# Kernel tuning notes

Measured on AMD Instinct MI355X. Metric: run time of the kernel, lower is better.

Reference implementation:

```python
import jax, jax.numpy as jnp
import numpy as np

B, N, F, H, D = 2, 2048, 1024, 16, 64


def setup_inputs() -> dict:
    key = jax.random.key(0)
    ks = jax.random.split(key, 5)
    s = 0.02
    return {
        "x": jax.random.normal(ks[0], (B, N, F), jnp.float32),
        "w_qkv": (jax.random.normal(ks[1], (3 * H * D, F), jnp.float32) * s),
        "w_out": (jax.random.normal(ks[2], (F, H * D), jnp.float32) * s),
        "w_hp_pre": (jax.random.normal(ks[3], (H, H), jnp.float32) * (1.0 / H)),
        "b_hp_pre": jnp.zeros((H,), jnp.float32),
        "w_hp_post": (jax.random.normal(ks[4], (H, H), jnp.float32) * (1.0 / H)),
        "b_hp_post": jnp.zeros((H,), jnp.float32),
    }


def reference(x, w_qkv, w_out, w_hp_pre, b_hp_pre, w_hp_post, b_hp_post):
    b, n, f = x.shape
    # qkv projection; rearrange 'b n (h d qkv) -> qkv b h n d' (qkv innermost)
    proj = (x @ w_qkv.T).reshape(b, n, H, D, 3)
    q = jnp.transpose(proj[..., 0], (0, 2, 1, 3))  # b h n d
    k = jnp.transpose(proj[..., 1], (0, 2, 1, 3))
    v = jnp.transpose(proj[..., 2], (0, 2, 1, 3))
    kv = jnp.stack([k, v], axis=0)  # (2, b, h, n, d) -- returned cache

    scale = D ** -0.5
    dots = jnp.einsum('bhid,bhjd->bhij', q, k) * scale
    # pre talking-heads: 1x1 conv over head channel
    dots = jnp.einsum('gh,bhij->bgij', w_hp_pre, dots) + b_hp_pre[None, :, None, None]
    attn = jax.nn.softmax(dots, axis=-1)
    # post talking-heads
    attn = jnp.einsum('gh,bhij->bgij', w_hp_post, attn) + b_hp_post[None, :, None, None]
    out = jnp.einsum('bhij,bhjd->bhid', attn, v)
    out = jnp.transpose(out, (0, 2, 1, 3)).reshape(b, n, H * D)
    out = out @ w_out.T
    return out, kv
```

## Files before the change

kernel.cpp:

```cpp
#include <hip/hip_runtime.h>
#include <hip/hip_bf16.h>
#include <cstdint>
#include <cstddef>

#define B_ 2
#define N_ 2048
#define F_ 1024
#define H_ 16
#define D_ 64

typedef float f32x4 __attribute__((ext_vector_type(4)));
typedef short s16x8 __attribute__((ext_vector_type(8)));
typedef short s16x4 __attribute__((ext_vector_type(4)));

__device__ __forceinline__ unsigned short f2bf(float f) {
  union { __hip_bfloat16 h; unsigned short u; } c;
  c.h = __float2bfloat16(f);
  return c.u;
}

__device__ __forceinline__ void bar_lgkm() {
  asm volatile("s_waitcnt lgkmcnt(0)" ::: "memory");
  __builtin_amdgcn_s_barrier();
}

__global__ __launch_bounds__(256) void cvt_bf16(const float* __restrict__ in,
                                                unsigned short* __restrict__ out,
                                                int n8) {
  const int t = blockIdx.x * 256 + threadIdx.x;
  if (t >= n8) return;
  const float4* p = (const float4*)in + (size_t)t * 2;
  float4 a = p[0], b = p[1];
  s16x8 o;
  o[0] = f2bf(a.x); o[1] = f2bf(a.y); o[2] = f2bf(a.z); o[3] = f2bf(a.w);
  o[4] = f2bf(b.x); o[5] = f2bf(b.y); o[6] = f2bf(b.z); o[7] = f2bf(b.w);
  *((s16x8*)out + t) = o;
}

__global__ __launch_bounds__(256) void cvt_wqkv_perm(const float* __restrict__ in,
                                                     unsigned short* __restrict__ out) {
  const int t = blockIdx.x * 256 + threadIdx.x;
  const int rowp = t >> 7;
  const int kk = (t & 127) * 8;
  const int c = rowp >> 10, rem = rowp & 1023;
  const int h = rem >> 6, d = rem & 63;
  const float* p = in + (size_t)(h * 192 + d * 3 + c) * 1024 + kk;
  float4 a = *(const float4*)p, b = *(const float4*)(p + 4);
  s16x8 o;
  o[0] = f2bf(a.x); o[1] = f2bf(a.y); o[2] = f2bf(a.z); o[3] = f2bf(a.w);
  o[4] = f2bf(b.x); o[5] = f2bf(b.y); o[6] = f2bf(b.z); o[7] = f2bf(b.w);
  *((s16x8*)&out[(size_t)rowp * 1024 + kk]) = o;
}

__global__ __launch_bounds__(256) void cvt_sum4(const float* __restrict__ a,
                                                unsigned short* __restrict__ out) {
  const int t = blockIdx.x * 256 + threadIdx.x;
  const size_t stride = (size_t)B_ * N_ * 1024 / 4;
  float4 x0 = *((const float4*)a + t);
  float4 x1 = *((const float4*)a + stride + t);
  float4 x2 = *((const float4*)a + 2 * stride + t);
  float4 x3 = *((const float4*)a + 3 * stride + t);
  s16x4 o;
  o[0] = f2bf((x0.x + x1.x) + (x2.x + x3.x));
  o[1] = f2bf((x0.y + x1.y) + (x2.y + x3.y));
  o[2] = f2bf((x0.z + x1.z) + (x2.z + x3.z));
  o[3] = f2bf((x0.w + x1.w) + (x2.w + x3.w));
  *((s16x4*)out + t) = o;
}

template <int MODE>
__global__ __launch_bounds__(256) void gemm_bf16(const unsigned short* __restrict__ A,
                                                 const unsigned short* __restrict__ W,
                                                 float* __restrict__ o0,
                                                 unsigned short* __restrict__ oQ,
                                                 unsigned short* __restrict__ oK,
                                                 unsigned short* __restrict__ oVt) {
  __shared__ unsigned short As[128 * 72];
  __shared__ unsigned short Bs[128 * 72];
  const int m0 = blockIdx.y * 128, c0 = blockIdx.x * 128;
  const int tid = threadIdx.x;
  const int wave = tid >> 6, lane = tid & 63;
  const int wm = (wave & 1) * 64, wn = (wave >> 1) * 64;
  const int lm = lane & 15, lq = lane >> 4;
  f32x4 acc[4][4] = {};
  for (int k0 = 0; k0 < 1024; k0 += 64) {
#pragma unroll
    for (int it = 0; it < 4; ++it) {
      const int chunk = it * 256 + tid;
      const int row = chunk >> 3, kq = (chunk & 7) * 8;
      *(float4*)&As[row * 72 + kq] = *(const float4*)&A[(size_t)(m0 + row) * 1024 + k0 + kq];
      *(float4*)&Bs[row * 72 + kq] = *(const float4*)&W[(size_t)(c0 + row) * 1024 + k0 + kq];
    }
    __syncthreads();
#pragma unroll
    for (int ks = 0; ks < 2; ++ks) {
      s16x8 af[4], bfr[4];
#pragma unroll
      for (int i = 0; i < 4; ++i) {
        af[i] = *(const s16x8*)&As[(wm + i * 16 + lm) * 72 + ks * 32 + lq * 8];
        bfr[i] = *(const s16x8*)&Bs[(wn + i * 16 + lm) * 72 + ks * 32 + lq * 8];
      }
#pragma unroll
      for (int i = 0; i < 4; ++i)
#pragma unroll
        for (int j = 0; j < 4; ++j)
          acc[i][j] = __builtin_amdgcn_mfma_f32_16x16x32_bf16(af[i], bfr[j], acc[i][j], 0, 0, 0);
    }
    __syncthreads();
  }
  if (MODE == 1) {
#pragma unroll
    for (int i = 0; i < 4; ++i)
#pragma unroll
      for (int j = 0; j < 4; ++j)
#pragma unroll
        for (int r = 0; r < 4; ++r) {
          const int m = m0 + wm + i * 16 + lq * 4 + r;
          const int col = c0 + wn + j * 16 + lm;
          o0[(size_t)m * 1024 + col] = acc[i][j][r];
        }
  } else {
    const int cls = blockIdx.x >> 3;
    const int colbase = (blockIdx.x & 7) * 128;
    if (cls == 0) {
#pragma unroll
      for (int i = 0; i < 4; ++i)
#pragma unroll
        for (int j = 0; j < 4; ++j) {
          const int cl = colbase + wn + j * 16 + lm;
          const int h = cl >> 6, d = cl & 63;
#pragma unroll
          for (int r = 0; r < 4; ++r) {
            const int m = m0 + wm + i * 16 + lq * 4 + r;
            const int bb = m >> 11, n = m & 2047;
            oQ[(((size_t)bb * H_ + h) * N_ + n) * D_ + d] = f2bf(acc[i][j][r]);
          }
        }
    } else if (cls == 1) {
#pragma unroll
      for (int i = 0; i < 4; ++i)
#pragma unroll
        for (int j = 0; j < 4; ++j) {
          const int cl = colbase + wn + j * 16 + lm;
          const int h = cl >> 6, d = cl & 63;
#pragma unroll
          for (int r = 0; r < 4; ++r) {
            const int m = m0 + wm + i * 16 + lq * 4 + r;
            const int bb = m >> 11, n = m & 2047;
            const size_t idx = (((size_t)bb * H_ + h) * N_ + n) * D_ + d;
            o0[idx] = acc[i][j][r];
            oK[idx] = f2bf(acc[i][j][r]);
          }
        }
    } else {
#pragma unroll
      for (int i = 0; i < 4; ++i) {
        const int n0 = m0 + wm + i * 16 + lq * 4;
        const int bb = n0 >> 11, nl = n0 & 2047;
#pragma unroll
        for (int j = 0; j < 4; ++j) {
          const int cl = colbase + wn + j * 16 + lm;
          const int h = cl >> 6, d = cl & 63;
          s16x4 vp;
#pragma unroll
          for (int r = 0; r < 4; ++r) {
            const size_t idx = (((size_t)bb * H_ + h) * N_ + nl + r) * D_ + d;
            o0[(size_t)B_ * H_ * N_ * D_ + idx] = acc[i][j][r];
            vp[r] = (short)f2bf(acc[i][j][r]);
          }
          *(s16x4*)&oVt[(((size_t)bb * H_ + h) * D_ + d) * N_ + nl] = vp;
        }
      }
    }
  }
}

#define SS_J 20
#define SLOT 320
#define SS_I 644
#define SS_TOT (32 * SS_I + 16)
#define PS_J 36
#define PS_G 1156

__global__ __launch_bounds__(512, 4) void attn_l(const unsigned short* __restrict__ Qb,
                                                 const unsigned short* __restrict__ Kb,
                                                 const float* __restrict__ wpre,
                                                 const float* __restrict__ bpre,
                                                 float* __restrict__ l_glob) {
  __shared__ unsigned short Ssh[SS_TOT];
  const int tid = threadIdx.x;
  const int wave = tid >> 6, lane = tid & 63;
  const int lm = lane & 15, lq = lane >> 4;
  const int b = blockIdx.z, jh = blockIdx.y;
  const int i0 = blockIdx.x * 32;
  const int j00 = jh * 512;
  const int h0 = wave * 2;

  for (int t = tid; t < SS_TOT; t += 512) Ssh[t] = 0;

  s16x8 aq[2][2][2];
#pragma unroll
  for (int hh = 0; hh < 2; ++hh)
#pragma unroll
    for (int mi = 0; mi < 2; ++mi)
#pragma unroll
      for (int ks = 0; ks < 2; ++ks)
        aq[hh][mi][ks] = *(const s16x8*)&Qb[(((size_t)(b * H_ + h0 + hh) * N_) + i0 + mi * 16 + lm) * D_ + ks * 32 + lq * 8];

  s16x8 apre;
#pragma unroll
  for (int t = 0; t < 8; ++t) apre[t] = 0;
  if (lq < 2)
#pragma unroll
    for (int t = 0; t < 8; ++t) apre[t] = (short)f2bf(wpre[lm * 16 + lq * 8 + t] * 0.125f);
  float bpre_r[4];
#pragma unroll
  for (int r = 0; r < 4; ++r) bpre_r[r] = bpre[lq * 4 + r];

  float lacc[4][4] = {};

  for (int js = 0; js < 512; js += 32) {
    const int j0 = j00 + js;
    s16x8 kr[2][2][2];
#pragma unroll
    for (int jt = 0; jt < 2; ++jt)
#pragma unroll
      for (int hh = 0; hh < 2; ++hh) {
        const unsigned short* kp = &Kb[(((size_t)(b * H_ + h0 + hh) * N_) + j0 + jt * 16 + lm) * D_ + lq * 8];
        kr[jt][hh][0] = *(const s16x8*)kp;
        kr[jt][hh][1] = *(const s16x8*)(kp + 32);
      }
    bar_lgkm();
#pragma unroll
    for (int jt = 0; jt < 2; ++jt) {
      f32x4 c[2][2];
#pragma unroll
      for (int hh = 0; hh < 2; ++hh)
#pragma unroll
        for (int mi = 0; mi < 2; ++mi) {
          f32x4 cc = {};
          cc = __builtin_amdgcn_mfma_f32_16x16x32_bf16(aq[hh][mi][0], kr[jt][hh][0], cc, 0, 0, 0);
          cc = __builtin_amdgcn_mfma_f32_16x16x32_bf16(aq[hh][mi][1], kr[jt][hh][1], cc, 0, 0, 0);
          c[hh][mi] = cc;
        }
#pragma unroll
      for (int mi = 0; mi < 2; ++mi)
#pragma unroll
        for (int r = 0; r < 4; ++r) {
          unsigned int pk = (unsigned int)f2bf(c[0][mi][r]) | ((unsigned int)f2bf(c[1][mi][r]) << 16);
          *(unsigned int*)&Ssh[(mi * 16 + lq * 4 + r) * SS_I + jt * SLOT + lm * SS_J + h0] = pk;
        }
    }
    bar_lgkm();
#pragma unroll
    for (int jt = 0; jt < 2; ++jt) {
      s16x4 p0[4], p1[4];
#pragma unroll
      for (int u = 0; u < 4; ++u) {
        const unsigned short* srow = &Ssh[(wave * 4 + u) * SS_I + jt * SLOT + lm * SS_J + lq * 8];
        p0[u] = *(const s16x4*)srow;
        p1[u] = *(const s16x4*)(srow + 4);
      }
#pragma unroll
      for (int u = 0; u < 4; ++u) {
        s16x8 bs;
        bs[0] = p0[u][0]; bs[1] = p0[u][1]; bs[2] = p0[u][2]; bs[3] = p0[u][3];
        bs[4] = p1[u][0]; bs[5] = p1[u][1]; bs[6] = p1[u][2]; bs[7] = p1[u][3];
        f32x4 c = {};
        c = __builtin_amdgcn_mfma_f32_16x16x32_bf16(apre, bs, c, 0, 0, 0);
#pragma unroll
        for (int r = 0; r < 4; ++r) lacc[u][r] += __expf(c[r] + bpre_r[r]);
      }
    }
  }
#pragma unroll
  for (int ig = 0; ig < 4; ++ig)
#pragma unroll
    for (int r = 0; r < 4; ++r) {
      float v = lacc[ig][r];
      v += __shfl_xor(v, 1); v += __shfl_xor(v, 2);
      v += __shfl_xor(v, 4); v += __shfl_xor(v, 8);
      if (lm == 0)
        atomicAdd(&l_glob[((size_t)b * N_ + i0 + wave * 4 + ig) * H_ + lq * 4 + r], v);
    }
}

__global__ __launch_bounds__(512, 2) void attn_av(const unsigned short* __restrict__ Qb,
                                                  const unsigned short* __restrict__ Kb,
                                                  const unsigned short* __restrict__ Vt,
                                                  const float* __restrict__ wpre,
                                                  const float* __restrict__ bpre,
                                                  const float* __restrict__ wpost,
                                                  const float* __restrict__ bpost,
                                                  const float* __restrict__ l_glob,
                                                  float* __restrict__ Opart) {
  __shared__ unsigned short Ssh[SS_TOT];
  __shared__ unsigned short Psh[16 * PS_G];
  __shared__ float linv[512];
  const int tid = threadIdx.x;
  const int wave = tid >> 6, lane = tid & 63;
  const int lm = lane & 15, lq = lane >> 4;
  const int b = blockIdx.z, jh = blockIdx.y;
  const int i0 = blockIdx.x * 32;
  const int j00 = jh * 512;
  const int h0 = wave * 2;
  float* Oout = Opart + (size_t)jh * ((size_t)B_ * N_ * 1024);

  for (int t = tid; t < SS_TOT; t += 512) Ssh[t] = 0;
  linv[tid] = 1.0f / l_glob[((size_t)b * N_ + i0 + (tid >> 4)) * H_ + (tid & 15)];

  s16x8 aq[2][2][2];
#pragma unroll
  for (int hh = 0; hh < 2; ++hh)
#pragma unroll
    for (int mi = 0; mi < 2; ++mi)
#pragma unroll
      for (int ks = 0; ks < 2; ++ks)
        aq[hh][mi][ks] = *(const s16x8*)&Qb[(((size_t)(b * H_ + h0 + hh) * N_) + i0 + mi * 16 + lm) * D_ + ks * 32 + lq * 8];

  s16x8 apre, apost;
#pragma unroll
  for (int t = 0; t < 8; ++t) { apre[t] = 0; apost[t] = 0; }
  if (lq < 2)
#pragma unroll
    for (int t = 0; t < 8; ++t) {
      apre[t] = (short)f2bf(wpre[lm * 16 + lq * 8 + t] * 0.125f);
      apost[t] = (short)f2bf(wpost[lm * 16 + lq * 8 + t]);
    }
  float bpre_r[4];
#pragma unroll
  for (int r = 0; r < 4; ++r) bpre_r[r] = bpre[lq * 4 + r];
  const float bpost_lm = bpost[lm];

  __syncthreads();

  float lifs[4][4];
#pragma unroll
  for (int u = 0; u < 4; ++u)
#pragma unroll
    for (int r = 0; r < 4; ++r)
      lifs[u][r] = linv[(wave * 4 + u) * 16 + lq * 4 + r];

  f32x4 acc[2][2][4] = {};

  for (int js = 0; js < 512; js += 32) {
    const int j0 = j00 + js;
    s16x8 kr[2][2][2];
#pragma unroll
    for (int jt = 0; jt < 2; ++jt)
#pragma unroll
      for (int hh = 0; hh < 2; ++hh) {
        const unsigned short* kp = &Kb[(((size_t)(b * H_ + h0 + hh) * N_) + j0 + jt * 16 + lm) * D_ + lq * 8];
        kr[jt][hh][0] = *(const s16x8*)kp;
        kr[jt][hh][1] = *(const s16x8*)(kp + 32);
      }
    s16x8 vtreg[2][4];
#pragma unroll
    for (int g = 0; g < 2; ++g)
#pragma unroll
      for (int nd = 0; nd < 4; ++nd)
        vtreg[g][nd] = *(const s16x8*)&Vt[(((size_t)(b * H_ + h0 + g) * D_) + nd * 16 + lm) * N_ + j0 + lq * 8];
#pragma unroll
    for (int jt = 0; jt < 2; ++jt) {
      f32x4 c[2][2];
#pragma unroll
      for (int hh = 0; hh < 2; ++hh)
#pragma unroll
        for (int mi = 0; mi < 2; ++mi) {
          f32x4 cc = {};
          cc = __builtin_amdgcn_mfma_f32_16x16x32_bf16(aq[hh][mi][0], kr[jt][hh][0], cc, 0, 0, 0);
          cc = __builtin_amdgcn_mfma_f32_16x16x32_bf16(aq[hh][mi][1], kr[jt][hh][1], cc, 0, 0, 0);
          c[hh][mi] = cc;
        }
#pragma unroll
      for (int mi = 0; mi < 2; ++mi)
#pragma unroll
        for (int r = 0; r < 4; ++r) {
          unsigned int pk = (unsigned int)f2bf(c[0][mi][r]) | ((unsigned int)f2bf(c[1][mi][r]) << 16);
          *(unsigned int*)&Ssh[(mi * 16 + lq * 4 + r) * SS_I + jt * SLOT + lm * SS_J + h0] = pk;
        }
    }
    bar_lgkm();
#pragma unroll
    for (int jt = 0; jt < 2; ++jt) {
      s16x4 p0[4], p1[4];
#pragma unroll
      for (int u = 0; u < 4; ++u) {
        const unsigned short* srow = &Ssh[(wave * 4 + u) * SS_I + jt * SLOT + lm * SS_J + lq * 8];
        p0[u] = *(const s16x4*)srow;
        p1[u] = *(const s16x4*)(srow + 4);
      }
      f32x4 cpre[4];
#pragma unroll
      for (int u = 0; u < 4; ++u) {
        s16x8 bs;
        bs[0] = p0[u][0]; bs[1] = p0[u][1]; bs[2] = p0[u][2]; bs[3] = p0[u][3];
        bs[4] = p1[u][0]; bs[5] = p1[u][1]; bs[6] = p1[u][2]; bs[7] = p1[u][3];
        f32x4 c = {};
        cpre[u] = __builtin_amdgcn_mfma_f32_16x16x32_bf16(apre, bs, c, 0, 0, 0);
      }
#pragma unroll
      for (int u = 0; u < 4; ++u) {
        unsigned short* srow = &Ssh[(wave * 4 + u) * SS_I + jt * SLOT];
        s16x4 ep;
#pragma unroll
        for (int r = 0; r < 4; ++r)
          ep[r] = (short)f2bf(__expf(cpre[u][r] + bpre_r[r]) * lifs[u][r]);
        *(s16x4*)(srow + lm * SS_J + lq * 4) = ep;
      }
      s16x4 q0[4], q1[4];
#pragma unroll
      for (int u = 0; u < 4; ++u) {
        const unsigned short* srow = &Ssh[(wave * 4 + u) * SS_I + jt * SLOT + lm * SS_J + lq * 8];
        q0[u] = *(const s16x4*)srow;
        q1[u] = *(const s16x4*)(srow + 4);
      }
#pragma unroll
      for (int u = 0; u < 4; ++u) {
        s16x8 be;
        be[0] = q0[u][0]; be[1] = q0[u][1]; be[2] = q0[u][2]; be[3] = q0[u][3];
        be[4] = q1[u][0]; be[5] = q1[u][1]; be[6] = q1[u][2]; be[7] = q1[u][3];
        f32x4 c2 = {};
        c2 = __builtin_amdgcn_mfma_f32_16x16x32_bf16(be, apost, c2, 0, 0, 0);
        s16x4 pv;
#pragma unroll
        for (int r = 0; r < 4; ++r) pv[r] = (short)f2bf(c2[r] + bpost_lm);
        *(s16x4*)&Psh[lm * PS_G + (wave * 4 + u) * PS_J + jt * 16 + lq * 4] = pv;
      }
    }
    bar_lgkm();
    s16x8 ap[2][2];
#pragma unroll
    for (int g = 0; g < 2; ++g)
#pragma unroll
      for (int mi = 0; mi < 2; ++mi) {
        const unsigned short* pb = &Psh[(h0 + g) * PS_G + (mi * 16 + lm) * PS_J + lq * 8];
        s16x4 a0 = *(const s16x4*)pb;
        s16x4 a1 = *(const s16x4*)(pb + 4);
        s16x8 t;
        t[0] = a0[0]; t[1] = a0[1]; t[2] = a0[2]; t[3] = a0[3];
        t[4] = a1[0]; t[5] = a1[1]; t[6] = a1[2]; t[7] = a1[3];
        ap[g][mi] = t;
      }
#pragma unroll
    for (int g = 0; g < 2; ++g)
#pragma unroll
      for (int mi = 0; mi < 2; ++mi)
#pragma unroll
        for (int nd = 0; nd < 4; ++nd)
          acc[g][mi][nd] = __builtin_amdgcn_mfma_f32_16x16x32_bf16(ap[g][mi], vtreg[g][nd], acc[g][mi][nd], 0, 0, 0);
  }
#pragma unroll
  for (int g = 0; g < 2; ++g)
#pragma unroll
    for (int mi = 0; mi < 2; ++mi)
#pragma unroll
      for (int nd = 0; nd < 4; ++nd)
#pragma unroll
        for (int r = 0; r < 4; ++r)
          Oout[((size_t)b * N_ + i0 + mi * 16 + lq * 4 + r) * 1024 + (h0 + g) * 64 + nd * 16 + lm] = acc[g][mi][nd][r];
}

extern "C" void kernel_launch(void* const* d_in, const int* in_sizes, int n_in,
                              void* d_out, int out_size, void* d_ws,
                              size_t ws_size, hipStream_t stream) {
  (void)in_sizes; (void)n_in; (void)out_size; (void)ws_size;
  const float* x      = (const float*)d_in[0];
  const float* w_qkv  = (const float*)d_in[1];
  const float* w_out  = (const float*)d_in[2];
  const float* w_pre  = (const float*)d_in[3];
  const float* b_pre  = (const float*)d_in[4];
  const float* w_post = (const float*)d_in[5];
  const float* b_post = (const float*)d_in[6];

  float* out = (float*)d_out;
  float* kv  = out + (size_t)B_ * N_ * F_;

  unsigned short* xb  = (unsigned short*)d_ws;
  unsigned short* wqb = xb + (size_t)4096 * 1024;
  unsigned short* wob = wqb + (size_t)3072 * 1024;
  unsigned short* Qb  = wob + (size_t)1024 * 1024;
  unsigned short* Kb  = Qb + (size_t)B_ * H_ * N_ * D_;
  unsigned short* Vt  = Kb + (size_t)B_ * H_ * N_ * D_;
  unsigned short* O1  = Vt + (size_t)B_ * H_ * N_ * D_;
  float* l_glob = (float*)(O1 + (size_t)B_ * N_ * F_);
  float* Oh = l_glob + (size_t)B_ * N_ * H_;

  cvt_bf16<<<dim3(4096 * 1024 / 8 / 256), 256, 0, stream>>>(x, xb, 4096 * 1024 / 8);
  cvt_wqkv_perm<<<dim3(3072 * 128 / 256), 256, 0, stream>>>(w_qkv, wqb);
  cvt_bf16<<<dim3(1024 * 1024 / 8 / 256), 256, 0, stream>>>(w_out, wob, 1024 * 1024 / 8);
  hipMemsetAsync(l_glob, 0, (size_t)B_ * N_ * H_ * 4, stream);

  gemm_bf16<0><<<dim3(3072 / 128, 4096 / 128), 256, 0, stream>>>(xb, wqb, kv, Qb, Kb, Vt);

  attn_l<<<dim3(N_ / 32, 4, B_), 512, 0, stream>>>(Qb, Kb, w_pre, b_pre, l_glob);
  attn_av<<<dim3(N_ / 32, 4, B_), 512, 0, stream>>>(Qb, Kb, Vt, w_pre, b_pre, w_post, b_post,
                                                    l_glob, Oh);

  cvt_sum4<<<dim3(B_ * N_ * F_ / 4 / 256), 256, 0, stream>>>(Oh, O1);

  gemm_bf16<1><<<dim3(1024 / 128, 4096 / 128), 256, 0, stream>>>(O1, wob, out, nullptr, nullptr, nullptr);
}
```

Measured before the change: 411.4 us.

## Software-pipeline attention loops with double-buffered scores and register prefetch

Restructures both attention kernels so the next tile's K and V global loads are issued a step ahead into registers, and in attn_av the score phase for step t+1 is computed into a second LDS buffer while step t is consumed. This removes one barrier per iteration and hides global load latency. It also replaces the LDS write/read round trip for the exp values with ds_bpermute lane shuffles, and adds s_setprio around MFMA bursts. In exchange attn_av doubles its score and probability LDS buffers, which may lower occupancy, and register pressure rises from the prefetched tiles.

```diff
diff --git a/kernel.cpp b/kernel.cpp
--- a/kernel.cpp
+++ b/kernel.cpp
@@ -178,16 +178,73 @@
 #define SS_J 20
 #define SLOT 320
 #define SS_I 644
-#define SS_TOT (32 * SS_I + 16)
+#define SS_HALF (32 * SS_I + 16)
 #define PS_J 36
 #define PS_G 1156
+#define PS_HALF (16 * PS_G)
+
+__device__ __forceinline__ f32x4 mfma16(s16x8 a, s16x8 b, f32x4 c) {
+  return __builtin_amdgcn_mfma_f32_16x16x32_bf16(a, b, c, 0, 0, 0);
+}
+
+__device__ __forceinline__ void load_k(s16x8 (&kr)[2][2][2],
+                                       const unsigned short* __restrict__ Kb,
+                                       int b, int h0, int j0, int lm, int lq) {
+#pragma unroll
+  for (int jt = 0; jt < 2; ++jt)
+#pragma unroll
+    for (int hh = 0; hh < 2; ++hh) {
+      const unsigned short* kp =
+          &Kb[(((size_t)(b * H_ + h0 + hh) * N_) + j0 + jt * 16 + lm) * D_ + lq * 8];
+      kr[jt][hh][0] = *(const s16x8*)kp;
+      kr[jt][hh][1] = *(const s16x8*)(kp + 32);
+    }
+}
+
+__device__ __forceinline__ void load_v(s16x8 (&vt)[2][4],
+                                       const unsigned short* __restrict__ Vt,
+                                       int b, int h0, int j0, int lm, int lq) {
+#pragma unroll
+  for (int g = 0; g < 2; ++g)
+#pragma unroll
+    for (int nd = 0; nd < 4; ++nd)
+      vt[g][nd] = *(const s16x8*)&Vt[(((size_t)(b * H_ + h0 + g) * D_) + nd * 16 + lm) * N_ + j0 + lq * 8];
+}
+
+__device__ __forceinline__ void scores_phase(const s16x8 (&aq)[2][2][2],
+                                             const s16x8 (&kr)[2][2][2],
+                                             unsigned short* Sb,
+                                             int lm, int lq, int h0) {
+#pragma unroll
+  for (int jt = 0; jt < 2; ++jt) {
+    f32x4 c[2][2];
+    __builtin_amdgcn_s_setprio(1);
+#pragma unroll
+    for (int hh = 0; hh < 2; ++hh)
+#pragma unroll
+      for (int mi = 0; mi < 2; ++mi) {
+        f32x4 cc = {};
+        cc = mfma16(aq[hh][mi][0], kr[jt][hh][0], cc);
+        cc = mfma16(aq[hh][mi][1], kr[jt][hh][1], cc);
+        c[hh][mi] = cc;
+      }
+    __builtin_amdgcn_s_setprio(0);
+#pragma unroll
+    for (int mi = 0; mi < 2; ++mi)
+#pragma unroll
+      for (int r = 0; r < 4; ++r) {
+        unsigned int pk = (unsigned int)f2bf(c[0][mi][r]) | ((unsigned int)f2bf(c[1][mi][r]) << 16);
+        *(unsigned int*)&Sb[(mi * 16 + lq * 4 + r) * SS_I + jt * SLOT + lm * SS_J + h0] = pk;
+      }
+  }
+}
 
 __global__ __launch_bounds__(512, 4) void attn_l(const unsigned short* __restrict__ Qb,
                                                  const unsigned short* __restrict__ Kb,
                                                  const float* __restrict__ wpre,
                                                  const float* __restrict__ bpre,
                                                  float* __restrict__ l_glob) {
-  __shared__ unsigned short Ssh[SS_TOT];
+  __shared__ unsigned short Ssh[SS_HALF];
   const int tid = threadIdx.x;
   const int wave = tid >> 6, lane = tid & 63;
   const int lm = lane & 15, lq = lane >> 4;
@@ -196,7 +253,7 @@
   const int j00 = jh * 512;
   const int h0 = wave * 2;
 
-  for (int t = tid; t < SS_TOT; t += 512) Ssh[t] = 0;
+  for (int t = tid; t < SS_HALF; t += 512) Ssh[t] = 0;
 
   s16x8 aq[2][2][2];
 #pragma unroll
@@ -219,38 +276,14 @@
 
   float lacc[4][4] = {};
 
-  for (int js = 0; js < 512; js += 32) {
-    const int j0 = j00 + js;
-    s16x8 kr[2][2][2];
-#pragma unroll
-    for (int jt = 0; jt < 2; ++jt)
-#pragma unroll
-      for (int hh = 0; hh < 2; ++hh) {
-        const unsigned short* kp = &Kb[(((size_t)(b * H_ + h0 + hh) * N_) + j0 + jt * 16 + lm) * D_ + lq * 8];
-        kr[jt][hh][0] = *(const s16x8*)kp;
-        kr[jt][hh][1] = *(const s16x8*)(kp + 32);
-      }
+  s16x8 kr[2][2][2];
+  load_k(kr, Kb, b, h0, j00, lm, lq);
+
+  for (int t = 0; t < 16; ++t) {
     bar_lgkm();
-#pragma unroll
-    for (int jt = 0; jt < 2; ++jt) {
-      f32x4 c[2][2];
-#pragma unroll
-      for (int hh = 0; hh < 2; ++hh)
-#pragma unroll
-        for (int mi = 0; mi < 2; ++mi) {
-          f32x4 cc = {};
-          cc = __builtin_amdgcn_mfma_f32_16x16x32_bf16(aq[hh][mi][0], kr[jt][hh][0], cc, 0, 0, 0);
-          cc = __builtin_amdgcn_mfma_f32_16x16x32_bf16(aq[hh][mi][1], kr[jt][hh][1], cc, 0, 0, 0);
-          c[hh][mi] = cc;
-        }
-#pragma unroll
-      for (int mi = 0; mi < 2; ++mi)
-#pragma unroll
-        for (int r = 0; r < 4; ++r) {
-          unsigned int pk = (unsigned int)f2bf(c[0][mi][r]) | ((unsigned int)f2bf(c[1][mi][r]) << 16);
-          *(unsigned int*)&Ssh[(mi * 16 + lq * 4 + r) * SS_I + jt * SLOT + lm * SS_J + h0] = pk;
-        }
-    }
+    scores_phase(aq, kr, Ssh, lm, lq, h0);
+    const int jn = j00 + (t + 1 < 16 ? (t + 1) * 32 : 480);
+    load_k(kr, Kb, b, h0, jn, lm, lq);
     bar_lgkm();
 #pragma unroll
     for (int jt = 0; jt < 2; ++jt) {
@@ -267,7 +300,7 @@
         bs[0] = p0[u][0]; bs[1] = p0[u][1]; bs[2] = p0[u][2]; bs[3] = p0[u][3];
         bs[4] = p1[u][0]; bs[5] = p1[u][1]; bs[6] = p1[u][2]; bs[7] = p1[u][3];
         f32x4 c = {};
-        c = __builtin_amdgcn_mfma_f32_16x16x32_bf16(apre, bs, c, 0, 0, 0);
+        c = mfma16(apre, bs, c);
 #pragma unroll
         for (int r = 0; r < 4; ++r) lacc[u][r] += __expf(c[r] + bpre_r[r]);
       }
@@ -294,8 +327,8 @@
                                                   const float* __restrict__ bpost,
                                                   const float* __restrict__ l_glob,
                                                   float* __restrict__ Opart) {
-  __shared__ unsigned short Ssh[SS_TOT];
-  __shared__ unsigned short Psh[16 * PS_G];
+  __shared__ unsigned short Ssh[2 * SS_HALF];
+  __shared__ unsigned short Psh[2 * PS_HALF];
   __shared__ float linv[512];
   const int tid = threadIdx.x;
   const int wave = tid >> 6, lane = tid & 63;
@@ -306,7 +339,7 @@
   const int h0 = wave * 2;
   float* Oout = Opart + (size_t)jh * ((size_t)B_ * N_ * 1024);
 
-  for (int t = tid; t < SS_TOT; t += 512) Ssh[t] = 0;
+  for (int t = tid; t < 2 * SS_HALF; t += 512) Ssh[t] = 0;
   linv[tid] = 1.0f / l_glob[((size_t)b * N_ + i0 + (tid >> 4)) * H_ + (tid & 15)];
 
   s16x8 aq[2][2][2];
@@ -332,6 +365,9 @@
   for (int r = 0; r < 4; ++r) bpre_r[r] = bpre[lq * 4 + r];
   const float bpost_lm = bpost[lm];
 
+  const int bpA = ((((2 * lq) & 3) * 16 + lm) << 2);
+  const int bpB = ((((2 * lq + 1) & 3) * 16 + lm) << 2);
+
   __syncthreads();
 
   float lifs[4][4];
@@ -343,50 +379,24 @@
 
   f32x4 acc[2][2][4] = {};
 
-  for (int js = 0; js < 512; js += 32) {
-    const int j0 = j00 + js;
-    s16x8 kr[2][2][2];
-#pragma unroll
-    for (int jt = 0; jt < 2; ++jt)
-#pragma unroll
-      for (int hh = 0; hh < 2; ++hh) {
-        const unsigned short* kp = &Kb[(((size_t)(b * H_ + h0 + hh) * N_) + j0 + jt * 16 + lm) * D_ + lq * 8];
-        kr[jt][hh][0] = *(const s16x8*)kp;
-        kr[jt][hh][1] = *(const s16x8*)(kp + 32);
-      }
-    s16x8 vtreg[2][4];
-#pragma unroll
-    for (int g = 0; g < 2; ++g)
-#pragma unroll
-      for (int nd = 0; nd < 4; ++nd)
-        vtreg[g][nd] = *(const s16x8*)&Vt[(((size_t)(b * H_ + h0 + g) * D_) + nd * 16 + lm) * N_ + j0 + lq * 8];
-#pragma unroll
-    for (int jt = 0; jt < 2; ++jt) {
-      f32x4 c[2][2];
-#pragma unroll
-      for (int hh = 0; hh < 2; ++hh)
-#pragma unroll
-        for (int mi = 0; mi < 2; ++mi) {
-          f32x4 cc = {};
-          cc = __builtin_amdgcn_mfma_f32_16x16x32_bf16(aq[hh][mi][0], kr[jt][hh][0], cc, 0, 0, 0);
-          cc = __builtin_amdgcn_mfma_f32_16x16x32_bf16(aq[hh][mi][1], kr[jt][hh][1], cc, 0, 0, 0);
-          c[hh][mi] = cc;
-        }
-#pragma unroll
-      for (int mi = 0; mi < 2; ++mi)
-#pragma unroll
-        for (int r = 0; r < 4; ++r) {
-          unsigned int pk = (unsigned int)f2bf(c[0][mi][r]) | ((unsigned int)f2bf(c[1][mi][r]) << 16);
-          *(unsigned int*)&Ssh[(mi * 16 + lq * 4 + r) * SS_I + jt * SLOT + lm * SS_J + h0] = pk;
-        }
-    }
-    bar_lgkm();
+  s16x8 kr[2][2][2];
+  load_k(kr, Kb, b, h0, j00, lm, lq);
+  s16x8 vt[2][4];
+  load_v(vt, Vt, b, h0, j00, lm, lq);
+  scores_phase(aq, kr, &Ssh[0], lm, lq, h0);
+  load_k(kr, Kb, b, h0, j00 + 32, lm, lq);
+  bar_lgkm();
+
+#pragma unroll 2
+  for (int t = 0; t < 16; ++t) {
+    unsigned short* Sc = &Ssh[(t & 1) * SS_HALF];
+    unsigned short* Pc = &Psh[(t & 1) * PS_HALF];
 #pragma unroll
     for (int jt = 0; jt < 2; ++jt) {
       s16x4 p0[4], p1[4];
 #pragma unroll
       for (int u = 0; u < 4; ++u) {
-        const unsigned short* srow = &Ssh[(wave * 4 + u) * SS_I + jt * SLOT + lm * SS_J + lq * 8];
+        const unsigned short* srow = &Sc[(wave * 4 + u) * SS_I + jt * SLOT + lm * SS_J + lq * 8];
         p0[u] = *(const s16x4*)srow;
         p1[u] = *(const s16x4*)(srow + 4);
       }
@@ -397,36 +407,33 @@
         bs[0] = p0[u][0]; bs[1] = p0[u][1]; bs[2] = p0[u][2]; bs[3] = p0[u][3];
         bs[4] = p1[u][0]; bs[5] = p1[u][1]; bs[6] = p1[u][2]; bs[7] = p1[u][3];
         f32x4 c = {};
-        cpre[u] = __builtin_amdgcn_mfma_f32_16x16x32_bf16(apre, bs, c, 0, 0, 0);
+        cpre[u] = mfma16(apre, bs, c);
       }
 #pragma unroll
       for (int u = 0; u < 4; ++u) {
-        unsigned short* srow = &Ssh[(wave * 4 + u) * SS_I + jt * SLOT];
-        s16x4 ep;
-#pragma unroll
-        for (int r = 0; r < 4; ++r)
-          ep[r] = (short)f2bf(__expf(cpre[u][r] + bpre_r[r]) * lifs[u][r]);
-        *(s16x4*)(srow + lm * SS_J + lq * 4) = ep;
-      }
-      s16x4 q0[4], q1[4];
-#pragma unroll
-      for (int u = 0; u < 4; ++u) {
-        const unsigned short* srow = &Ssh[(wave * 4 + u) * SS_I + jt * SLOT + lm * SS_J + lq * 8];
-        q0[u] = *(const s16x4*)srow;
-        q1[u] = *(const s16x4*)(srow + 4);
-      }
-#pragma unroll
-      for (int u = 0; u < 4; ++u) {
-        s16x8 be;
-        be[0] = q0[u][0]; be[1] = q0[u][1]; be[2] = q0[u][2]; be[3] = q0[u][3];
-        be[4] = q1[u][0]; be[5] = q1[u][1]; be[6] = q1[u][2]; be[7] = q1[u][3];
+        float e0 = __expf(cpre[u][0] + bpre_r[0]) * lifs[u][0];
+        float e1 = __expf(cpre[u][1] + bpre_r[1]) * lifs[u][1];
+        float e2 = __expf(cpre[u][2] + bpre_r[2]) * lifs[u][2];
+        float e3 = __expf(cpre[u][3] + bpre_r[3]) * lifs[u][3];
+        int e01 = (int)((unsigned int)f2bf(e0) | ((unsigned int)f2bf(e1) << 16));
+        int e23 = (int)((unsigned int)f2bf(e2) | ((unsigned int)f2bf(e3) << 16));
+        union { int i[4]; s16x8 v; } cv;
+        cv.i[0] = __builtin_amdgcn_ds_bpermute(bpA, e01);
+        cv.i[1] = __builtin_amdgcn_ds_bpermute(bpA, e23);
+        cv.i[2] = __builtin_amdgcn_ds_bpermute(bpB, e01);
+        cv.i[3] = __builtin_amdgcn_ds_bpermute(bpB, e23);
         f32x4 c2 = {};
-        c2 = __builtin_amdgcn_mfma_f32_16x16x32_bf16(be, apost, c2, 0, 0, 0);
+        c2 = mfma16(cv.v, apost, c2);
         s16x4 pv;
 #pragma unroll
         for (int r = 0; r < 4; ++r) pv[r] = (short)f2bf(c2[r] + bpost_lm);
-        *(s16x4*)&Psh[lm * PS_G + (wave * 4 + u) * PS_J + jt * 16 + lq * 4] = pv;
-      }
+        *(s16x4*)&Pc[lm * PS_G + (wave * 4 + u) * PS_J + jt * 16 + lq * 4] = pv;
+      }
+    }
+    if (t < 15) {
+      scores_phase(aq, kr, &Ssh[((t + 1) & 1) * SS_HALF], lm, lq, h0);
+      const int jn = j00 + (t + 2 < 16 ? (t + 2) * 32 : 480);
+      load_k(kr, Kb, b, h0, jn, lm, lq);
     }
     bar_lgkm();
     s16x8 ap[2][2];
@@ -434,21 +441,25 @@
     for (int g = 0; g < 2; ++g)
 #pragma unroll
       for (int mi = 0; mi < 2; ++mi) {
-        const unsigned short* pb = &Psh[(h0 + g) * PS_G + (mi * 16 + lm) * PS_J + lq * 8];
+        const unsigned short* pb = &Pc[(h0 + g) * PS_G + (mi * 16 + lm) * PS_J + lq * 8];
         s16x4 a0 = *(const s16x4*)pb;
         s16x4 a1 = *(const s16x4*)(pb + 4);
-        s16x8 t;
-        t[0] = a0[0]; t[1] = a0[1]; t[2] = a0[2]; t[3] = a0[3];
-        t[4] = a1[0]; t[5] = a1[1]; t[6] = a1[2]; t[7] = a1[3];
-        ap[g][mi] = t;
-      }
+        s16x8 tt;
+        tt[0] = a0[0]; tt[1] = a0[1]; tt[2] = a0[2]; tt[3] = a0[3];
+        tt[4] = a1[0]; tt[5] = a1[1]; tt[6] = a1[2]; tt[7] = a1[3];
+        ap[g][mi] = tt;
+      }
+    __builtin_amdgcn_s_setprio(1);
 #pragma unroll
     for (int g = 0; g < 2; ++g)
 #pragma unroll
       for (int mi = 0; mi < 2; ++mi)
 #pragma unroll
         for (int nd = 0; nd < 4; ++nd)
-          acc[g][mi][nd] = __builtin_amdgcn_mfma_f32_16x16x32_bf16(ap[g][mi], vtreg[g][nd], acc[g][mi][nd], 0, 0, 0);
+          acc[g][mi][nd] = mfma16(ap[g][mi], vt[g][nd], acc[g][mi][nd]);
+    __builtin_amdgcn_s_setprio(0);
+    const int jv = j00 + (t + 1 < 16 ? (t + 1) * 32 : 480);
+    load_v(vt, Vt, b, h0, jv, lm, lq);
   }
 #pragma unroll
   for (int g = 0; g < 2; ++g)
```

Measured after the change: 383.8 us. -6.7%, faster.
